# Optimization experiments

Hardware: AMD Instinct MI355X
Metric: run time of the kernel (lower is better)

Reference implementation:

```python
import jax, jax.numpy as jnp
import numpy as np
from jax import lax

B, C, H, W = 8, 64, 256, 256
GROUPS, EPS = 8, 1e-5


def setup_inputs() -> dict:
    key = jax.random.key(0)
    ks = jax.random.split(key, 7)
    scale = 1.0 / np.sqrt(C)
    return {
        "x": jax.random.normal(ks[0], (B, C, H, W), dtype=jnp.float32),
        "gn_w": jnp.ones((C,), dtype=jnp.float32),
        "gn_b": jnp.zeros((C,), dtype=jnp.float32),
        "gate_w": jax.random.normal(ks[1], (C, C), dtype=jnp.float32) * scale,
        "gate_b": jnp.zeros((C,), dtype=jnp.float32),
        "upd_w": jax.random.normal(ks[2], (C, C), dtype=jnp.float32) * scale,
        "upd_b": jnp.zeros((C,), dtype=jnp.float32),
    }


def _group_norm(x, w, b):
    b_, c, h, wd = x.shape
    xg = x.reshape(b_, GROUPS, c // GROUPS, h, wd)
    mu = xg.mean(axis=(2, 3, 4), keepdims=True)
    var = xg.var(axis=(2, 3, 4), keepdims=True)
    xn = ((xg - mu) * lax.rsqrt(var + EPS)).reshape(b_, c, h, wd)
    return xn * w[None, :, None, None] + b[None, :, None, None]


def _gated_scan(gate_f, u_f):
    # gate_f, u_f: [T, ...]; s_t = g_t * s_{t-1} + (1 - g_t) * u_t, s_{-1} = 0
    def step(s, gu):
        g, u = gu
        s = g * s + (1.0 - g) * u
        return s, s
    _, ys = lax.scan(step, jnp.zeros_like(u_f[0]), (gate_f, u_f))
    return ys


def reference(x, gn_w, gn_b, gate_w, gate_b, upd_w, upd_b):
    h = _group_norm(x, gn_w, gn_b)
    # 1x1 convs as channel contractions
    gate = jax.nn.sigmoid(jnp.einsum('oc,bchw->bohw', gate_w, h) + gate_b[None, :, None, None])
    u = jnp.einsum('oc,bchw->bohw', upd_w, h) + upd_b[None, :, None, None]
    # column scan over W: carry [B, C, H]
    hw = _gated_scan(gate.transpose(3, 0, 1, 2), u.transpose(3, 0, 1, 2))  # [W,B,C,H]
    hw = hw.transpose(1, 2, 3, 0)  # [B,C,H,W]
    # row scan over H: carry [B, C, W]
    hh = _gated_scan(gate.transpose(2, 0, 1, 3), hw.transpose(2, 0, 1, 3))  # [H,B,C,W]
    hh = hh.transpose(1, 2, 0, 3)  # [B,C,H,W]
    return x + hh
```

## Files before the change

kernel.cpp:

```cpp
#include <hip/hip_runtime.h>
#include <stdint.h>

#define BB   8
#define CC   64
#define HH   256
#define WW   256
#define HWSZ (HH*WW)
#define CHW  (CC*HH*WW)
#define GROUPELEMS (8*HWSZ)
#define EPSV 1e-5f

#define WS_PART_OFF  0
#define WS_AFF_OFF   4096
#define WS_WFRAG_OFF 8192

typedef __attribute__((ext_vector_type(8))) short bf16x8;
typedef __attribute__((ext_vector_type(4))) float f32x4;
typedef __attribute__((ext_vector_type(4))) unsigned int u32x4;
union U32x4 { uint32_t u[4]; uint4 q; bf16x8 v; u32x4 nv; };

__device__ __forceinline__ uint32_t f32_to_bf16_bits(float f) {
    uint32_t u = __float_as_uint(f);
    u += 0x7fffu + ((u >> 16) & 1u);
    return u >> 16;
}

__global__ __launch_bounds__(256) void k_stats_partial(
        const float* __restrict__ x, float2* __restrict__ part,
        const float* __restrict__ gw, const float* __restrict__ uw,
        uint32_t* __restrict__ wfrag) {
    int blk = blockIdx.x;
    int t = threadIdx.x;
    if (blk < 16) {
        int idx = blk * 256 + t;
        int fi = idx >> 8, rem = idx & 255;
        int l = rem >> 2, d = rem & 3;
        int mt = fi >> 1, s = fi & 1;
        int m = 16 * mt + (l & 15);
        int k = 32 * s + 8 * (l >> 4) + 2 * d;
        const float* Wr = (m < 64) ? (gw + m * 64) : (uw + (m - 64) * 64);
        wfrag[idx] = f32_to_bf16_bits(Wr[k]) | (f32_to_bf16_bits(Wr[k + 1]) << 16);
    }
    const float4* p = (const float4*)(x + (size_t)blk * 65536);
    float s = 0.f, s2 = 0.f;
#pragma unroll 16
    for (int i = 0; i < 64; ++i) {
        float4 v = p[t + i * 256];
        s  += v.x + v.y + v.z + v.w;
        s2 += v.x * v.x + v.y * v.y + v.z * v.z + v.w * v.w;
    }
#pragma unroll
    for (int off = 32; off; off >>= 1) {
        s  += __shfl_down(s,  off, 64);
        s2 += __shfl_down(s2, off, 64);
    }
    __shared__ float2 red[4];
    int wid = t >> 6;
    if ((t & 63) == 0) red[wid] = make_float2(s, s2);
    __syncthreads();
    if (t == 0) {
        float a = 0.f, b2 = 0.f;
#pragma unroll
        for (int i = 0; i < 4; ++i) { a += red[i].x; b2 += red[i].y; }
        part[blk] = make_float2(a, b2);
    }
}

__global__ __launch_bounds__(512) void k_stats_final(
        const float2* __restrict__ part,
        const float* __restrict__ gn_w, const float* __restrict__ gn_b,
        float2* __restrict__ aff) {
    __shared__ float2 st[64];
    int t = threadIdx.x;
    if (t < 64) {
        float s = 0.f, s2 = 0.f;
#pragma unroll
        for (int i = 0; i < 8; ++i) { float2 p = part[t * 8 + i]; s += p.x; s2 += p.y; }
        float inv  = 1.0f / (float)GROUPELEMS;
        float mu   = s * inv;
        float var  = s2 * inv - mu * mu;
        st[t] = make_float2(mu, rsqrtf(var + EPSV));
    }
    __syncthreads();
    int b = t >> 6, c = t & 63, g = c >> 3;
    float2 mr = st[b * 8 + g];
    float a  = mr.y * gn_w[c];
    aff[t] = make_float2(a, gn_b[c] - mr.x * a);
}

__global__ __launch_bounds__(256, 4) void k_row(
        const float* __restrict__ x,
        const uint32_t* __restrict__ wfrag,
        const float* __restrict__ gate_b, const float* __restrict__ upd_b,
        const float2* __restrict__ aff,
        uint32_t* __restrict__ pair) {
    __shared__ uint32_t gvhn[128 * 65];
    __shared__ float2 affs[64];
    __shared__ __align__(16) float bgs[64];
    __shared__ __align__(16) float bus[64];

    const int t = threadIdx.x;
    const int w = t >> 6, l = t & 63, q = l >> 4, r16 = l & 15;
    const int row = blockIdx.x;
    const int b = row >> 8, y = row & 255;
    const size_t rowoff = (size_t)b * CHW + (size_t)y * WW;

    if (t < 64) { affs[t] = aff[b * 64 + t]; bgs[t] = gate_b[t]; bus[t] = upd_b[t]; }

    bf16x8 A[8][2];
#pragma unroll
    for (int mt = 0; mt < 8; ++mt)
#pragma unroll
        for (int s = 0; s < 2; ++s) {
            U32x4 u;
            u.q = *(const uint4*)(wfrag + (((mt << 1) | s) * 64 + l) * 4);
            A[mt][s] = u.v;
        }
    __syncthreads();

    float s_carry = 0.f;
    for (int tau = 0; tau < 2; ++tau) {
        const int x0 = tau << 7;
#pragma unroll
        for (int i = 0; i < 4; ++i) {
            int unit = i * 256 + t;
            int c2 = unit >> 5, p4 = unit & 31;
            int c = c2 << 1, px = p4 << 2;
            const float* xp = x + rowoff + (size_t)c * HWSZ + x0 + px;
            float4 v0 = *(const float4*)xp;
            float4 v1 = *(const float4*)(xp + HWSZ);
            float2 a0 = affs[c], a1 = affs[c + 1];
            uint32_t base = px * 65 + c2;
            gvhn[base]       = f32_to_bf16_bits(v0.x * a0.x + a0.y)
                             | (f32_to_bf16_bits(v1.x * a1.x + a1.y) << 16);
            gvhn[base + 65]  = f32_to_bf16_bits(v0.y * a0.x + a0.y)
                             | (f32_to_bf16_bits(v1.y * a1.x + a1.y) << 16);
            gvhn[base + 130] = f32_to_bf16_bits(v0.z * a0.x + a0.y)
                             | (f32_to_bf16_bits(v1.z * a1.x + a1.y) << 16);
            gvhn[base + 195] = f32_to_bf16_bits(v0.w * a0.x + a0.y)
                             | (f32_to_bf16_bits(v1.w * a1.x + a1.y) << 16);
        }
        __syncthreads();

#pragma unroll
        for (int nc = 0; nc < 2; ++nc) {
            int n_local = (w << 5) + (nc << 4) + r16;
            int based = n_local * 65 + 4 * q;
            U32x4 B0u, B1u;
#pragma unroll
            for (int d = 0; d < 4; ++d) B0u.u[d] = gvhn[based + d];
#pragma unroll
            for (int d = 0; d < 4; ++d) B1u.u[d] = gvhn[based + 16 + d];
            f32x4 acc[8];
#pragma unroll
            for (int mt = 0; mt < 4; ++mt) {
                acc[mt]     = *(const f32x4*)(bgs + 16 * mt + 4 * q);
                acc[mt + 4] = *(const f32x4*)(bus + 16 * mt + 4 * q);
            }
#pragma unroll
            for (int mt = 0; mt < 8; ++mt)
                acc[mt] = __builtin_amdgcn_mfma_f32_16x16x32_bf16(A[mt][0], B0u.v, acc[mt], 0, 0, 0);
#pragma unroll
            for (int mt = 0; mt < 8; ++mt)
                acc[mt] = __builtin_amdgcn_mfma_f32_16x16x32_bf16(A[mt][1], B1u.v, acc[mt], 0, 0, 0);
#pragma unroll
            for (int mt = 0; mt < 4; ++mt)
#pragma unroll
                for (int r = 0; r < 4; ++r) {
                    float ga = acc[mt][r];
                    float ua = acc[mt + 4][r];
                    float g  = 1.0f / (1.0f + __expf(-ga));
                    float vv = (1.0f - g) * ua;
                    uint32_t pk = __builtin_amdgcn_perm(__float_as_uint(vv),
                                                        __float_as_uint(g), 0x07060302u);
                    gvhn[n_local * 65 + 16 * mt + 4 * q + r] = pk;
                }
        }
        __syncthreads();

        if (t < 64) {
            float s = s_carry;
#pragma unroll 8
            for (int xi = 0; xi < 128; ++xi) {
                uint32_t pk = gvhn[xi * 65 + t];
                float g = __uint_as_float(pk << 16);
                float v = __uint_as_float(pk & 0xffff0000u);
                s = __builtin_fmaf(g, s, v);
                gvhn[xi * 65 + t] = __builtin_amdgcn_perm(__float_as_uint(s), pk, 0x07060100u);
            }
            s_carry = s;
        }
        __syncthreads();

#pragma unroll
        for (int i = 0; i < 8; ++i) {
            int unit = i * 256 + t;
            int c = unit >> 5, p4 = unit & 31;
            int px = p4 << 2;
            uint32_t bidx = px * 65 + c;
            u32x4 o;
            o.x = gvhn[bidx];
            o.y = gvhn[bidx + 65];
            o.z = gvhn[bidx + 130];
            o.w = gvhn[bidx + 195];
            __builtin_nontemporal_store(o,
                (u32x4*)(pair + rowoff + (size_t)c * HWSZ + x0 + px));
        }
        __syncthreads();
    }
}

__global__ __launch_bounds__(256) void k_hscan(
        uint32_t* __restrict__ io, const float* __restrict__ x) {
    int t = threadIdx.x;
    size_t base = (size_t)blockIdx.x * HWSZ + t;
    uint32_t pk[16]; float xv[16];
#pragma unroll
    for (int j = 0; j < 16; ++j) pk[j] = __builtin_nontemporal_load(io + base + (size_t)j * WW);
#pragma unroll
    for (int j = 0; j < 16; ++j) xv[j] = __builtin_nontemporal_load(x + base + (size_t)j * WW);
    float s = 0.f;
    for (int yt = 0; yt < 16; ++yt) {
        uint32_t npk[16]; float nxv[16];
        if (yt < 15) {
            size_t nb = base + (size_t)(yt + 1) * 16 * WW;
#pragma unroll
            for (int j = 0; j < 16; ++j) npk[j] = __builtin_nontemporal_load(io + nb + (size_t)j * WW);
#pragma unroll
            for (int j = 0; j < 16; ++j) nxv[j] = __builtin_nontemporal_load(x + nb + (size_t)j * WW);
        }
        float gj[16], vj[16];
#pragma unroll
        for (int j = 0; j < 16; ++j) {
            float g   = __uint_as_float(pk[j] << 16);
            float hwv = __uint_as_float(pk[j] & 0xffff0000u);
            gj[j] = g; vj[j] = (1.f - g) * hwv;
        }
        float res[16];
#pragma unroll
        for (int j = 0; j < 16; ++j) { s = __builtin_fmaf(gj[j], s, vj[j]); res[j] = xv[j] + s; }
        size_t ob = base + (size_t)yt * 16 * WW;
#pragma unroll
        for (int j = 0; j < 16; ++j)
            __builtin_nontemporal_store(__float_as_uint(res[j]), io + ob + (size_t)j * WW);
#pragma unroll
        for (int j = 0; j < 16; ++j) { pk[j] = npk[j]; xv[j] = nxv[j]; }
    }
}

extern "C" void kernel_launch(void* const* d_in, const int* in_sizes, int n_in,
                              void* d_out, int out_size, void* d_ws, size_t ws_size,
                              hipStream_t stream) {
    const float* x      = (const float*)d_in[0];
    const float* gn_w   = (const float*)d_in[1];
    const float* gn_b   = (const float*)d_in[2];
    const float* gate_w = (const float*)d_in[3];
    const float* gate_b = (const float*)d_in[4];
    const float* upd_w  = (const float*)d_in[5];
    const float* upd_b  = (const float*)d_in[6];

    char* ws = (char*)d_ws;
    float2*   part  = (float2*)(ws + WS_PART_OFF);
    float2*   aff   = (float2*)(ws + WS_AFF_OFF);
    uint32_t* wfrag = (uint32_t*)(ws + WS_WFRAG_OFF);
    uint32_t* pair  = (uint32_t*)d_out;

    k_stats_partial<<<512, 256, 0, stream>>>(x, part, gate_w, upd_w, wfrag);
    k_stats_final<<<1, 512, 0, stream>>>(part, gn_w, gn_b, aff);
    k_row<<<BB * HH, 256, 0, stream>>>(x, wfrag, gate_b, upd_b, aff, pair);
    k_hscan<<<BB * CC, 256, 0, stream>>>(pair, x);
}
```

Before: 396.7 us.

## Split H-direction scan into segmented aggregate/fix/apply passes for more parallelism

Replaces the single-pass row scan (512 blocks, each serially scanning 256 rows) with a three-kernel segmented scan: per-segment aggregation of the gate product and partial state, a small carry-fix pass, then an apply pass over 2048 blocks. The goal is to raise occupancy and memory-level parallelism for the latency-bound serial scan. In exchange the packed gate/value buffer is read an extra time and two more launches are added. It also moves the weight-fragment loads in k_row out of persistent registers into per-iteration loads, to reduce register pressure at the cost of repeated global/cache reads.

```diff
diff --git a/kernel.cpp b/kernel.cpp
--- a/kernel.cpp
+++ b/kernel.cpp
@@ -10,9 +10,12 @@
 #define GROUPELEMS (8*HWSZ)
 #define EPSV 1e-5f
 
-#define WS_PART_OFF  0
-#define WS_AFF_OFF   4096
-#define WS_WFRAG_OFF 8192
+#define WS_PART_OFF   0
+#define WS_AFF_OFF    4096
+#define WS_WFRAG_OFF  8192
+#define WS_CARRY_OFF  32768
+#define WS_SIN_OFF    4227072
+#define WS_NEED       6324224
 
 typedef __attribute__((ext_vector_type(8))) short bf16x8;
 typedef __attribute__((ext_vector_type(4))) float f32x4;
@@ -106,16 +109,6 @@
     const size_t rowoff = (size_t)b * CHW + (size_t)y * WW;
 
     if (t < 64) { affs[t] = aff[b * 64 + t]; bgs[t] = gate_b[t]; bus[t] = upd_b[t]; }
-
-    bf16x8 A[8][2];
-#pragma unroll
-    for (int mt = 0; mt < 8; ++mt)
-#pragma unroll
-        for (int s = 0; s < 2; ++s) {
-            U32x4 u;
-            u.q = *(const uint4*)(wfrag + (((mt << 1) | s) * 64 + l) * 4);
-            A[mt][s] = u.v;
-        }
     __syncthreads();
 
     float s_carry = 0.f;
@@ -157,12 +150,17 @@
                 acc[mt]     = *(const f32x4*)(bgs + 16 * mt + 4 * q);
                 acc[mt + 4] = *(const f32x4*)(bus + 16 * mt + 4 * q);
             }
-#pragma unroll
-            for (int mt = 0; mt < 8; ++mt)
-                acc[mt] = __builtin_amdgcn_mfma_f32_16x16x32_bf16(A[mt][0], B0u.v, acc[mt], 0, 0, 0);
-#pragma unroll
-            for (int mt = 0; mt < 8; ++mt)
-                acc[mt] = __builtin_amdgcn_mfma_f32_16x16x32_bf16(A[mt][1], B1u.v, acc[mt], 0, 0, 0);
+            uintptr_t wfa = (uintptr_t)wfrag;
+            asm volatile("" : "+s"(wfa));
+            const uint32_t* wf = (const uint32_t*)wfa;
+#pragma unroll
+            for (int mt = 0; mt < 8; ++mt) {
+                U32x4 a0, a1;
+                a0.q = *(const uint4*)(wf + (((mt << 1) | 0) * 64 + l) * 4);
+                a1.q = *(const uint4*)(wf + (((mt << 1) | 1) * 64 + l) * 4);
+                acc[mt] = __builtin_amdgcn_mfma_f32_16x16x32_bf16(a0.v, B0u.v, acc[mt], 0, 0, 0);
+                acc[mt] = __builtin_amdgcn_mfma_f32_16x16x32_bf16(a1.v, B1u.v, acc[mt], 0, 0, 0);
+            }
 #pragma unroll
             for (int mt = 0; mt < 4; ++mt)
 #pragma unroll
@@ -210,6 +208,89 @@
     }
 }
 
+
+__global__ __launch_bounds__(256) void k_hseg_agg(
+        const uint32_t* __restrict__ io, float2* __restrict__ carry) {
+    int blk = blockIdx.x;
+    int t = threadIdx.x;
+    size_t base = (size_t)(blk >> 2) * HWSZ + (size_t)(blk & 3) * 64 * WW + t;
+    float G = 1.f, V = 0.f;
+    uint32_t pk[16];
+#pragma unroll
+    for (int j = 0; j < 16; ++j) pk[j] = io[base + (size_t)j * WW];
+    for (int grp = 0; grp < 4; ++grp) {
+        uint32_t npk[16];
+        if (grp < 3) {
+            size_t nb = base + (size_t)(grp + 1) * 16 * WW;
+#pragma unroll
+            for (int j = 0; j < 16; ++j) npk[j] = io[nb + (size_t)j * WW];
+        }
+#pragma unroll
+        for (int j = 0; j < 16; ++j) {
+            float g  = __uint_as_float(pk[j] << 16);
+            float hw = __uint_as_float(pk[j] & 0xffff0000u);
+            V = __builtin_fmaf(g, V, (1.f - g) * hw);
+            G *= g;
+        }
+#pragma unroll
+        for (int j = 0; j < 16; ++j) pk[j] = npk[j];
+    }
+    carry[(size_t)blk * 256 + t] = make_float2(G, V);
+}
+
+__global__ __launch_bounds__(256) void k_hseg_fix(
+        const float2* __restrict__ carry, float* __restrict__ sin_) {
+    int t = threadIdx.x;
+    size_t cb = (size_t)blockIdx.x * 1024 + t;
+    float s = 0.f;
+#pragma unroll
+    for (int seg = 0; seg < 4; ++seg) {
+        sin_[cb + seg * 256] = s;
+        float2 gv = carry[cb + seg * 256];
+        s = __builtin_fmaf(gv.x, s, gv.y);
+    }
+}
+
+__global__ __launch_bounds__(256) void k_hseg_apply(
+        uint32_t* __restrict__ io, const float* __restrict__ x,
+        const float* __restrict__ sin_) {
+    int blk = blockIdx.x;
+    int t = threadIdx.x;
+    size_t base = (size_t)(blk >> 2) * HWSZ + (size_t)(blk & 3) * 64 * WW + t;
+    float s = sin_[(size_t)blk * 256 + t];
+    uint32_t pk[16]; float xv[16];
+#pragma unroll
+    for (int j = 0; j < 16; ++j) pk[j] = __builtin_nontemporal_load(io + base + (size_t)j * WW);
+#pragma unroll
+    for (int j = 0; j < 16; ++j) xv[j] = __builtin_nontemporal_load(x + base + (size_t)j * WW);
+    for (int grp = 0; grp < 4; ++grp) {
+        uint32_t npk[16]; float nxv[16];
+        if (grp < 3) {
+            size_t nb = base + (size_t)(grp + 1) * 16 * WW;
+#pragma unroll
+            for (int j = 0; j < 16; ++j) npk[j] = __builtin_nontemporal_load(io + nb + (size_t)j * WW);
+#pragma unroll
+            for (int j = 0; j < 16; ++j) nxv[j] = __builtin_nontemporal_load(x + nb + (size_t)j * WW);
+        }
+        float gj[16], vj[16];
+#pragma unroll
+        for (int j = 0; j < 16; ++j) {
+            float g   = __uint_as_float(pk[j] << 16);
+            float hwv = __uint_as_float(pk[j] & 0xffff0000u);
+            gj[j] = g; vj[j] = (1.f - g) * hwv;
+        }
+        float res[16];
+#pragma unroll
+        for (int j = 0; j < 16; ++j) { s = __builtin_fmaf(gj[j], s, vj[j]); res[j] = xv[j] + s; }
+        size_t ob = base + (size_t)grp * 16 * WW;
+#pragma unroll
+        for (int j = 0; j < 16; ++j)
+            __builtin_nontemporal_store(__float_as_uint(res[j]), io + ob + (size_t)j * WW);
+#pragma unroll
+        for (int j = 0; j < 16; ++j) { pk[j] = npk[j]; xv[j] = nxv[j]; }
+    }
+}
+
 __global__ __launch_bounds__(256) void k_hscan(
         uint32_t* __restrict__ io, const float* __restrict__ x) {
     int t = threadIdx.x;
@@ -268,5 +349,14 @@
     k_stats_partial<<<512, 256, 0, stream>>>(x, part, gate_w, upd_w, wfrag);
     k_stats_final<<<1, 512, 0, stream>>>(part, gn_w, gn_b, aff);
     k_row<<<BB * HH, 256, 0, stream>>>(x, wfrag, gate_b, upd_b, aff, pair);
-    k_hscan<<<BB * CC, 256, 0, stream>>>(pair, x);
-}
+
+    if (ws_size >= (size_t)WS_NEED) {
+        float2* carry = (float2*)(ws + WS_CARRY_OFF);
+        float*  sin_  = (float*)(ws + WS_SIN_OFF);
+        k_hseg_agg<<<BB * CC * 4, 256, 0, stream>>>(pair, carry);
+        k_hseg_fix<<<BB * CC, 256, 0, stream>>>(carry, sin_);
+        k_hseg_apply<<<BB * CC * 4, 256, 0, stream>>>(pair, x, sin_);
+    } else {
+        k_hscan<<<BB * CC, 256, 0, stream>>>(pair, x);
+    }
+}
```

After: 386.8 us. -2.5%, faster.

## Split H-scan into 4 segments per column with two-pass carry combine

Applied to the files above, without the earlier changes.

The vertical scan kernel now uses 1024 threads per (b,c) plane. Each column is cut into four 64-row segments: a first pass computes each segment's composed (G,V) affine summary, a shared-memory prefix combines the segment carries, and a second pass rescans to write outputs. This exposes four times more parallelism than the old single 256-row sequential chain, at the cost of reading the packed gate/value data twice. The row kernel also drops register-held A fragments in favour of per-MFMA loads from wfrag, to lower register pressure. It switches the pair stores and loads from nontemporal to regular so the intermediate can stay in cache for the rereads.

```diff
diff --git a/kernel.cpp b/kernel.cpp
--- a/kernel.cpp
+++ b/kernel.cpp
@@ -10,9 +10,9 @@
 #define GROUPELEMS (8*HWSZ)
 #define EPSV 1e-5f
 
-#define WS_PART_OFF  0
-#define WS_AFF_OFF   4096
-#define WS_WFRAG_OFF 8192
+#define WS_PART_OFF   0
+#define WS_AFF_OFF    4096
+#define WS_WFRAG_OFF  8192
 
 typedef __attribute__((ext_vector_type(8))) short bf16x8;
 typedef __attribute__((ext_vector_type(4))) float f32x4;
@@ -106,16 +106,6 @@
     const size_t rowoff = (size_t)b * CHW + (size_t)y * WW;
 
     if (t < 64) { affs[t] = aff[b * 64 + t]; bgs[t] = gate_b[t]; bus[t] = upd_b[t]; }
-
-    bf16x8 A[8][2];
-#pragma unroll
-    for (int mt = 0; mt < 8; ++mt)
-#pragma unroll
-        for (int s = 0; s < 2; ++s) {
-            U32x4 u;
-            u.q = *(const uint4*)(wfrag + (((mt << 1) | s) * 64 + l) * 4);
-            A[mt][s] = u.v;
-        }
     __syncthreads();
 
     float s_carry = 0.f;
@@ -157,12 +147,17 @@
                 acc[mt]     = *(const f32x4*)(bgs + 16 * mt + 4 * q);
                 acc[mt + 4] = *(const f32x4*)(bus + 16 * mt + 4 * q);
             }
-#pragma unroll
-            for (int mt = 0; mt < 8; ++mt)
-                acc[mt] = __builtin_amdgcn_mfma_f32_16x16x32_bf16(A[mt][0], B0u.v, acc[mt], 0, 0, 0);
-#pragma unroll
-            for (int mt = 0; mt < 8; ++mt)
-                acc[mt] = __builtin_amdgcn_mfma_f32_16x16x32_bf16(A[mt][1], B1u.v, acc[mt], 0, 0, 0);
+            uintptr_t wfa = (uintptr_t)wfrag;
+            asm volatile("" : "+s"(wfa));
+            const uint32_t* wf = (const uint32_t*)wfa;
+#pragma unroll
+            for (int mt = 0; mt < 8; ++mt) {
+                U32x4 a0, a1;
+                a0.q = *(const uint4*)(wf + (((mt << 1) | 0) * 64 + l) * 4);
+                a1.q = *(const uint4*)(wf + (((mt << 1) | 1) * 64 + l) * 4);
+                acc[mt] = __builtin_amdgcn_mfma_f32_16x16x32_bf16(a0.v, B0u.v, acc[mt], 0, 0, 0);
+                acc[mt] = __builtin_amdgcn_mfma_f32_16x16x32_bf16(a1.v, B1u.v, acc[mt], 0, 0, 0);
+            }
 #pragma unroll
             for (int mt = 0; mt < 4; ++mt)
 #pragma unroll
@@ -203,46 +198,71 @@
             o.y = gvhn[bidx + 65];
             o.z = gvhn[bidx + 130];
             o.w = gvhn[bidx + 195];
-            __builtin_nontemporal_store(o,
-                (u32x4*)(pair + rowoff + (size_t)c * HWSZ + x0 + px));
-        }
-        __syncthreads();
-    }
-}
-
-__global__ __launch_bounds__(256) void k_hscan(
+            *(u32x4*)(pair + rowoff + (size_t)c * HWSZ + x0 + px) = o;
+        }
+        __syncthreads();
+    }
+}
+
+__global__ __launch_bounds__(1024) void k_hscan2(
         uint32_t* __restrict__ io, const float* __restrict__ x) {
-    int t = threadIdx.x;
-    size_t base = (size_t)blockIdx.x * HWSZ + t;
+    __shared__ float2 gvs[4][256];
+    __shared__ float  sins[4][256];
+    const int t = threadIdx.x;
+    const int col = t & 255, seg = t >> 8;
+    const size_t base = (size_t)blockIdx.x * HWSZ + (size_t)seg * 64 * WW + col;
+
+    float G = 1.f, V = 0.f;
+    for (int grp = 0; grp < 4; ++grp) {
+        uint32_t pk[16];
+        size_t gb = base + (size_t)grp * 16 * WW;
+#pragma unroll
+        for (int j = 0; j < 16; ++j) pk[j] = io[gb + (size_t)j * WW];
+#pragma unroll
+        for (int j = 0; j < 16; ++j) {
+            float g  = __uint_as_float(pk[j] << 16);
+            float hw = __uint_as_float(pk[j] & 0xffff0000u);
+            V = __builtin_fmaf(g, V, (1.f - g) * hw);
+            G *= g;
+        }
+    }
+    gvs[seg][col] = make_float2(G, V);
+    __syncthreads();
+
+    if (t < 256) {
+        float s = 0.f;
+#pragma unroll
+        for (int sg = 0; sg < 4; ++sg) {
+            sins[sg][t] = s;
+            float2 gv = gvs[sg][t];
+            s = __builtin_fmaf(gv.x, s, gv.y);
+        }
+    }
+    __syncthreads();
+
+    float s = sins[seg][col];
     uint32_t pk[16]; float xv[16];
 #pragma unroll
-    for (int j = 0; j < 16; ++j) pk[j] = __builtin_nontemporal_load(io + base + (size_t)j * WW);
+    for (int j = 0; j < 16; ++j) pk[j] = io[base + (size_t)j * WW];
 #pragma unroll
     for (int j = 0; j < 16; ++j) xv[j] = __builtin_nontemporal_load(x + base + (size_t)j * WW);
-    float s = 0.f;
-    for (int yt = 0; yt < 16; ++yt) {
+    for (int grp = 0; grp < 4; ++grp) {
         uint32_t npk[16]; float nxv[16];
-        if (yt < 15) {
-            size_t nb = base + (size_t)(yt + 1) * 16 * WW;
-#pragma unroll
-            for (int j = 0; j < 16; ++j) npk[j] = __builtin_nontemporal_load(io + nb + (size_t)j * WW);
+        if (grp < 3) {
+            size_t nb = base + (size_t)(grp + 1) * 16 * WW;
+#pragma unroll
+            for (int j = 0; j < 16; ++j) npk[j] = io[nb + (size_t)j * WW];
 #pragma unroll
             for (int j = 0; j < 16; ++j) nxv[j] = __builtin_nontemporal_load(x + nb + (size_t)j * WW);
         }
-        float gj[16], vj[16];
+        size_t ob = base + (size_t)grp * 16 * WW;
 #pragma unroll
         for (int j = 0; j < 16; ++j) {
             float g   = __uint_as_float(pk[j] << 16);
             float hwv = __uint_as_float(pk[j] & 0xffff0000u);
-            gj[j] = g; vj[j] = (1.f - g) * hwv;
-        }
-        float res[16];
-#pragma unroll
-        for (int j = 0; j < 16; ++j) { s = __builtin_fmaf(gj[j], s, vj[j]); res[j] = xv[j] + s; }
-        size_t ob = base + (size_t)yt * 16 * WW;
-#pragma unroll
-        for (int j = 0; j < 16; ++j)
-            __builtin_nontemporal_store(__float_as_uint(res[j]), io + ob + (size_t)j * WW);
+            s = __builtin_fmaf(g, s, (1.f - g) * hwv);
+            __builtin_nontemporal_store(__float_as_uint(xv[j] + s), io + ob + (size_t)j * WW);
+        }
 #pragma unroll
         for (int j = 0; j < 16; ++j) { pk[j] = npk[j]; xv[j] = nxv[j]; }
     }
@@ -268,5 +288,5 @@
     k_stats_partial<<<512, 256, 0, stream>>>(x, part, gate_w, upd_w, wfrag);
     k_stats_final<<<1, 512, 0, stream>>>(part, gn_w, gn_b, aff);
     k_row<<<BB * HH, 256, 0, stream>>>(x, wfrag, gate_b, upd_b, aff, pair);
-    k_hscan<<<BB * CC, 256, 0, stream>>>(pair, x);
-}
+    k_hscan2<<<BB * CC, 1024, 0, stream>>>(pair, x);
+}
```

Result: faster. 360.6 us (-9.1%).
